# Kernel optimization log

Measured on AMD Instinct MI355X. Metric: run time of the kernel, lower is better.

The kernel has to match this reference:

```python
import jax, jax.numpy as jnp
import numpy as np

N = 100000
E = 1600000
IN_DIM = 64
H_DIM = 64
OUT_DIM = 1


def gcn_conv(x, edge_index, W, b):
    """PyG-style GCNConv: D^-1/2 (A + I) D^-1/2 X W + b."""
    n = x.shape[0]
    h = x @ W  # [N, h]
    src, dst = edge_index[0], edge_index[1]
    # degree with self-loops
    deg = jax.ops.segment_sum(jnp.ones(src.shape[0], x.dtype), dst, num_segments=n) + 1.0
    dinv = jax.lax.rsqrt(deg)  # deg >= 1 always (self-loops)
    # neighbor messages, symmetric normalization
    coef = dinv[src] * dinv[dst]                       # [E]
    msg = h[src] * coef[:, None]                       # [E, h]
    agg = jax.ops.segment_sum(msg, dst, num_segments=n)
    # self-loop contribution
    agg = agg + h * (dinv * dinv)[:, None]
    return agg + b


def setup_inputs() -> dict:
    key = jax.random.key(0)
    ks = jax.random.split(key, 14)
    s = lambda d: 1.0 / np.sqrt(d)
    return {
        "x": jax.random.normal(ks[0], (N, IN_DIM), jnp.float32),
        "edge_index": jax.random.randint(ks[1], (2, E), 0, N, jnp.int64),
        "fake_x": jax.random.normal(ks[2], (N, IN_DIM), jnp.float32),
        "fake_edge_index": jax.random.randint(ks[3], (2, E), 0, N, jnp.int64),
        "W1": jax.random.uniform(ks[4], (IN_DIM, H_DIM), jnp.float32, -s(IN_DIM), s(IN_DIM)),
        "b1": jnp.zeros((H_DIM,), jnp.float32),
        "W2": jax.random.uniform(ks[5], (H_DIM, H_DIM), jnp.float32, -s(H_DIM), s(H_DIM)),
        "b2": jnp.zeros((H_DIM,), jnp.float32),
        "Wy": jax.random.uniform(ks[6], (H_DIM, OUT_DIM), jnp.float32, -s(H_DIM), s(H_DIM)),
        "by": jnp.zeros((OUT_DIM,), jnp.float32),
        "Wp": jax.random.uniform(ks[7], (H_DIM, OUT_DIM), jnp.float32, -s(H_DIM), s(H_DIM)),
        "bp": jnp.zeros((OUT_DIM,), jnp.float32),
        "Wb": jax.random.uniform(ks[8], (H_DIM, OUT_DIM), jnp.float32, -s(H_DIM), s(H_DIM)),
        "bb": jnp.zeros((OUT_DIM,), jnp.float32),
    }


def reference(x, edge_index, fake_x, fake_edge_index,
              W1, b1, W2, b2, Wy, by, Wp, bp, Wb, bb):
    # eval mode: dropout is identity
    xZ1 = jax.nn.relu(gcn_conv(x, edge_index, W1, b1))
    xfZ1 = jax.nn.relu(gcn_conv(fake_x, fake_edge_index, W1, b1))
    xZ2 = gcn_conv(xZ1, edge_index, W2, b2)
    xfZ2 = gcn_conv(xfZ1, fake_edge_index, W2, b2)
    yi = jax.nn.relu(xZ2 @ Wy + by)
    fprob = jax.nn.relu(xZ2 @ Wp + bp)
    fprob_f = jax.nn.relu(xfZ2 @ Wp + bp)
    treat_prob = jax.nn.relu(xZ2 @ Wb + bb)
    return (yi, fprob, fprob_f, treat_prob)
```

## Files before the change

kernel.cpp:

```cpp
#include <hip/hip_runtime.h>
#include <hip/hip_bf16.h>

typedef __hip_bfloat16 bf16;

__device__ __forceinline__ float b2f(bf16 v) { return __bfloat162float(v); }
__device__ __forceinline__ float bu2f(unsigned short u) { return __uint_as_float(((unsigned)u) << 16); }
__device__ __forceinline__ unsigned short f2bu(float f) {
    bf16 h = __float2bfloat16(f);
    return *(unsigned short*)&h;
}

__device__ __forceinline__ int getIdx(const void* p, long long i, int is64) {
    return is64 ? (int)(((const long long*)p)[i]) : ((const int*)p)[i];
}
__device__ __forceinline__ float loadF(const void* p, size_t i, int isF32) {
    return isF32 ? ((const float*)p)[i] : b2f(((const bf16*)p)[i]);
}
__device__ __forceinline__ void storeF(void* p, size_t i, float v, int isF32) {
    if (isF32) ((float*)p)[i] = v;
    else       ((bf16*)p)[i]  = __float2bfloat16(v);
}

#define NPART 128
#define CHUNK 2048
#define BINCAP 40
#define MAXSLICE 800

__global__ void setup_kernel(const void* __restrict__ edge, const void* __restrict__ x,
                             const void* __restrict__ b2, const void* __restrict__ W2,
                             const void* __restrict__ Wy, const void* __restrict__ by,
                             const void* __restrict__ Wp, const void* __restrict__ bp,
                             const void* __restrict__ Wb, const void* __restrict__ bb,
                             float* __restrict__ c, int* __restrict__ flags,
                             int* __restrict__ bCntAll) {
    __shared__ int sh_isF32;
    const int tid  = threadIdx.x;
    const int lane = tid & 63;
    const int wv   = tid >> 6;
    bCntAll[tid] = 0;
    if (wv == 0) {
        const int* e32 = (const int*)edge;
        int nz = 0;
        for (int k = 1 + 2 * lane; k < 1024; k += 128) nz |= (e32[k] != 0);
        int allzero = !__any(nz);
        if (allzero) {
            int nz2 = 0;
            for (int k = 1000001 + 2 * lane; k < 1002048; k += 128) nz2 |= (e32[k] != 0);
            allzero = !__any(nz2);
        }
        const unsigned short* u = (const unsigned short*)x;
        int insane = 0;
        for (int k = 2 * lane; k < 512; k += 128) {
            int ex = (u[k] >> 7) & 0xFF;
            if (ex != 0 && (ex < 90 || ex > 160)) insane++;
        }
#pragma unroll
        for (int off = 32; off > 0; off >>= 1) insane += __shfl_xor(insane, off, 64);
        if (lane == 0) {
            flags[0] = allzero;
            flags[1] = (insane > 64) ? 1 : 0;
            sh_isF32 = (insane > 64) ? 1 : 0;
        }
    }
    __syncthreads();
    const int isF32 = sh_isF32;
    if (wv == 0) {
        float b = loadF(b2, lane, isF32);
        float cy = b * loadF(Wy, lane, isF32);
        float cp = b * loadF(Wp, lane, isF32);
        float cb = b * loadF(Wb, lane, isF32);
#pragma unroll
        for (int off = 32; off > 0; off >>= 1) {
            cy += __shfl_xor(cy, off, 64);
            cp += __shfl_xor(cp, off, 64);
            cb += __shfl_xor(cb, off, 64);
        }
        if (lane == 0) {
            c[0] = cy + loadF(by, 0, isF32);
            c[1] = cp + loadF(bp, 0, isF32);
            c[2] = cb + loadF(bb, 0, isF32);
        }
    } else {
        const void* Wh = (wv == 1) ? Wy : (wv == 2) ? Wp : Wb;
        float* dst = c + 16 + (wv - 1) * 64;
        float acc = 0.f;
        for (int j = 0; j < 64; ++j)
            acc = fmaf(loadF(W2, (size_t)lane * 64 + j, isF32), loadF(Wh, j, isF32), acc);
        dst[lane] = acc;
    }
}

__global__ void bucket_kernel(const void* __restrict__ e0, const void* __restrict__ e1,
                              int E, int N,
                              unsigned* __restrict__ bk0, unsigned* __restrict__ bk1,
                              int bucketCap, int* __restrict__ bCntBase,
                              const int* __restrict__ flags) {
    __shared__ unsigned bins[NPART][BINCAP];
    __shared__ int binCnt[NPART];
    __shared__ int binBase[NPART];
    const int g = blockIdx.y;
    const void* edge = g ? e1 : e0;
    unsigned* __restrict__ bucket = g ? bk1 : bk0;
    int* __restrict__ bCnt = bCntBase + g * NPART;
    const int is64 = flags[0];
    const int tid = threadIdx.x;
    long long base = (long long)blockIdx.x * CHUNK;
    if (base >= E) return;
    if (tid < NPART) binCnt[tid] = 0;
    __syncthreads();
    for (int k = tid; k < CHUNK; k += 256) {
        long long e = base + k;
        if (e < E) {
            int s = getIdx(edge, e, is64);
            int d = getIdx(edge, (long long)E + e, is64);
            int p = (int)(((long long)d * NPART) / N);
            if (p > NPART - 1) p = NPART - 1;
            int lo = (int)(((long long)N * p + NPART - 1) / NPART);
            unsigned packed = ((unsigned)s << 10) | (unsigned)(d - lo);
            int idx = atomicAdd(&binCnt[p], 1);
            if (idx < BINCAP) bins[p][idx] = packed;
            else {
                int pos = atomicAdd(&bCnt[p], 1);
                bucket[(size_t)p * bucketCap + pos] = packed;
            }
        }
    }
    __syncthreads();
    if (tid < NPART) {
        int cnt = min(binCnt[tid], BINCAP);
        binBase[tid] = atomicAdd(&bCnt[tid], cnt);
        binCnt[tid]  = cnt;
    }
    __syncthreads();
    for (int p = 0; p < NPART; ++p) {
        int cnt = binCnt[p];
        int gb  = binBase[p];
        unsigned* dstp = bucket + (size_t)p * bucketCap + gb;
        for (int k = tid; k < cnt; k += 256) dstp[k] = bins[p][k];
    }
}

__global__ void csr_build_kernel(const unsigned* __restrict__ bk0, const unsigned* __restrict__ bk1,
                                 int bucketCap, const int* __restrict__ bCntBase,
                                 int* __restrict__ rp0, int* __restrict__ rp1,
                                 float* __restrict__ dv0, float* __restrict__ dv1,
                                 int* __restrict__ cs0, int* __restrict__ cs1,
                                 int N, int E) {
    __shared__ int hist[MAXSLICE];
    __shared__ int tmp[1024];
    __shared__ int partBase;
    const int g = blockIdx.y;
    const unsigned* __restrict__ bucket = g ? bk1 : bk0;
    const int* __restrict__ bCnt = bCntBase + g * NPART;
    int*   __restrict__ rowptr  = g ? rp1 : rp0;
    float* __restrict__ dinv    = g ? dv1 : dv0;
    int*   __restrict__ csr_src = g ? cs1 : cs0;
    const int tid = threadIdx.x;
    const int p  = blockIdx.x;
    const int lo = (int)(((long long)N * p + NPART - 1) / NPART);
    const int hi = (int)(((long long)N * (p + 1) + NPART - 1) / NPART);
    const int nloc = hi - lo;
    const int cnt = bCnt[p];
    for (int t = tid; t < nloc; t += 1024) hist[t] = 0;
    if (tid == 0) {
        int b = 0;
        for (int q = 0; q < p; ++q) b += bCnt[q];
        partBase = b;
    }
    __syncthreads();
    const unsigned* __restrict__ seg = bucket + (size_t)p * bucketCap;
    for (int e = tid; e < cnt; e += 1024) atomicAdd(&hist[seg[e] & 1023u], 1);
    __syncthreads();
    const int k0 = tid * 2;
    const int s0 = (k0     < nloc) ? hist[k0]     : 0;
    const int s1 = (k0 + 1 < nloc) ? hist[k0 + 1] : 0;
    tmp[tid] = s0 + s1;
    __syncthreads();
#pragma unroll
    for (int off = 1; off < 1024; off <<= 1) {
        int v = (tid >= off) ? tmp[tid - off] : 0;
        __syncthreads();
        tmp[tid] += v;
        __syncthreads();
    }
    const int r0 = partBase + tmp[tid] - (s0 + s1);
    if (k0 < nloc) {
        rowptr[lo + k0] = r0;
        dinv[lo + k0]   = rsqrtf((float)s0 + 1.0f);
        hist[k0] = r0;
    }
    if (k0 + 1 < nloc) {
        rowptr[lo + k0 + 1] = r0 + s0;
        dinv[lo + k0 + 1]   = rsqrtf((float)s1 + 1.0f);
        hist[k0 + 1] = r0 + s0;
    }
    if (p == NPART - 1 && tid == 0) rowptr[N] = E;
    __syncthreads();
    int e = tid;
    for (; e + 3 * 1024 < cnt; e += 4 * 1024) {
        unsigned v0 = seg[e];
        unsigned v1 = seg[e + 1024];
        unsigned v2 = seg[e + 2048];
        unsigned v3 = seg[e + 3072];
        csr_src[atomicAdd(&hist[v0 & 1023u], 1)] = (int)(v0 >> 10);
        csr_src[atomicAdd(&hist[v1 & 1023u], 1)] = (int)(v1 >> 10);
        csr_src[atomicAdd(&hist[v2 & 1023u], 1)] = (int)(v2 >> 10);
        csr_src[atomicAdd(&hist[v3 & 1023u], 1)] = (int)(v3 >> 10);
    }
    for (; e < cnt; e += 1024) {
        unsigned v = seg[e];
        csr_src[atomicAdd(&hist[v & 1023u], 1)] = (int)(v >> 10);
    }
}

#define XSTR 68

__global__ void gemm64_kernel(const void* __restrict__ in0, const void* __restrict__ in1,
                              const void* __restrict__ W,
                              const float* __restrict__ dv0, const float* __restrict__ dv1,
                              unsigned short* __restrict__ o0, unsigned short* __restrict__ o1,
                              int N, const int* __restrict__ flags) {
    __shared__ float Wl[64 * 64];
    __shared__ float Xl[64 * XSTR];
    const int g = blockIdx.y;
    const void* __restrict__ in = g ? in1 : in0;
    const float* __restrict__ dinv = g ? dv1 : dv0;
    unsigned short* __restrict__ out = g ? o1 : o0;
    const int isF32 = flags[1];
    const int tid = threadIdx.x;
    if (isF32) {
        const float4* W4 = (const float4*)W;
        float4* Wl4 = (float4*)Wl;
        for (int t = tid; t < 64 * 16; t += 256) Wl4[t] = W4[t];
    } else {
        for (int t = tid; t < 64 * 64; t += 256) Wl[t] = b2f(((const bf16*)W)[t]);
    }
    const int lane = tid & 63;
    const int wave = tid >> 6;
    const int slot = lane >> 4;
    const int fi   = lane & 15;
    const int r0   = wave * 16 + slot;

    for (int base = blockIdx.x * 64; base < N; base += gridDim.x * 64) {
        __syncthreads();
        if (isF32) {
            const float4* in4 = (const float4*)in;
            for (int t = tid; t < 64 * 16; t += 256) {
                int r = t >> 4, c4 = t & 15;
                int gr = base + r;
                float4 v = (gr < N) ? in4[(size_t)gr * 16 + c4] : make_float4(0.f, 0.f, 0.f, 0.f);
                *(float4*)&Xl[r * XSTR + c4 * 4] = v;
            }
        } else {
            for (int t = tid; t < 64 * 64; t += 256) {
                int r = t >> 6, c = t & 63;
                int gr = base + r;
                Xl[r * XSTR + c] = (gr < N) ? b2f(((const bf16*)in)[(size_t)gr * 64 + c]) : 0.f;
            }
        }
        __syncthreads();

        float4 a0 = make_float4(0.f,0.f,0.f,0.f), a1 = a0, a2 = a0, a3 = a0;
#pragma unroll 2
        for (int k = 0; k < 64; k += 4) {
            float4 w0 = *(const float4*)&Wl[(k + 0) * 64 + fi * 4];
            float4 w1 = *(const float4*)&Wl[(k + 1) * 64 + fi * 4];
            float4 w2 = *(const float4*)&Wl[(k + 2) * 64 + fi * 4];
            float4 w3 = *(const float4*)&Wl[(k + 3) * 64 + fi * 4];
            float4 x0 = *(const float4*)&Xl[(r0 +  0) * XSTR + k];
            float4 x1 = *(const float4*)&Xl[(r0 +  4) * XSTR + k];
            float4 x2 = *(const float4*)&Xl[(r0 +  8) * XSTR + k];
            float4 x3 = *(const float4*)&Xl[(r0 + 12) * XSTR + k];
            a0.x=fmaf(x0.x,w0.x,a0.x); a0.y=fmaf(x0.x,w0.y,a0.y); a0.z=fmaf(x0.x,w0.z,a0.z); a0.w=fmaf(x0.x,w0.w,a0.w);
            a0.x=fmaf(x0.y,w1.x,a0.x); a0.y=fmaf(x0.y,w1.y,a0.y); a0.z=fmaf(x0.y,w1.z,a0.z); a0.w=fmaf(x0.y,w1.w,a0.w);
            a0.x=fmaf(x0.z,w2.x,a0.x); a0.y=fmaf(x0.z,w2.y,a0.y); a0.z=fmaf(x0.z,w2.z,a0.z); a0.w=fmaf(x0.z,w2.w,a0.w);
            a0.x=fmaf(x0.w,w3.x,a0.x); a0.y=fmaf(x0.w,w3.y,a0.y); a0.z=fmaf(x0.w,w3.z,a0.z); a0.w=fmaf(x0.w,w3.w,a0.w);
            a1.x=fmaf(x1.x,w0.x,a1.x); a1.y=fmaf(x1.x,w0.y,a1.y); a1.z=fmaf(x1.x,w0.z,a1.z); a1.w=fmaf(x1.x,w0.w,a1.w);
            a1.x=fmaf(x1.y,w1.x,a1.x); a1.y=fmaf(x1.y,w1.y,a1.y); a1.z=fmaf(x1.y,w1.z,a1.z); a1.w=fmaf(x1.y,w1.w,a1.w);
            a1.x=fmaf(x1.z,w2.x,a1.x); a1.y=fmaf(x1.z,w2.y,a1.y); a1.z=fmaf(x1.z,w2.z,a1.z); a1.w=fmaf(x1.z,w2.w,a1.w);
            a1.x=fmaf(x1.w,w3.x,a1.x); a1.y=fmaf(x1.w,w3.y,a1.y); a1.z=fmaf(x1.w,w3.z,a1.z); a1.w=fmaf(x1.w,w3.w,a1.w);
            a2.x=fmaf(x2.x,w0.x,a2.x); a2.y=fmaf(x2.x,w0.y,a2.y); a2.z=fmaf(x2.x,w0.z,a2.z); a2.w=fmaf(x2.x,w0.w,a2.w);
            a2.x=fmaf(x2.y,w1.x,a2.x); a2.y=fmaf(x2.y,w1.y,a2.y); a2.z=fmaf(x2.y,w1.z,a2.z); a2.w=fmaf(x2.y,w1.w,a2.w);
            a2.x=fmaf(x2.z,w2.x,a2.x); a2.y=fmaf(x2.z,w2.y,a2.y); a2.z=fmaf(x2.z,w2.z,a2.z); a2.w=fmaf(x2.z,w2.w,a2.w);
            a2.x=fmaf(x2.w,w3.x,a2.x); a2.y=fmaf(x2.w,w3.y,a2.y); a2.z=fmaf(x2.w,w3.z,a2.z); a2.w=fmaf(x2.w,w3.w,a2.w);
            a3.x=fmaf(x3.x,w0.x,a3.x); a3.y=fmaf(x3.x,w0.y,a3.y); a3.z=fmaf(x3.x,w0.z,a3.z); a3.w=fmaf(x3.x,w0.w,a3.w);
            a3.x=fmaf(x3.y,w1.x,a3.x); a3.y=fmaf(x3.y,w1.y,a3.y); a3.z=fmaf(x3.y,w1.z,a3.z); a3.w=fmaf(x3.y,w1.w,a3.w);
            a3.x=fmaf(x3.z,w2.x,a3.x); a3.y=fmaf(x3.z,w2.y,a3.y); a3.z=fmaf(x3.z,w2.z,a3.z); a3.w=fmaf(x3.z,w2.w,a3.w);
            a3.x=fmaf(x3.w,w3.x,a3.x); a3.y=fmaf(x3.w,w3.y,a3.y); a3.z=fmaf(x3.w,w3.z,a3.z); a3.w=fmaf(x3.w,w3.w,a3.w);
        }
        float4 acc[4] = {a0, a1, a2, a3};
#pragma unroll
        for (int j = 0; j < 4; ++j) {
            int r = base + r0 + 4 * j;
            if (r < N) {
                float d = dinv[r];
                ushort4 o;
                o.x = f2bu(acc[j].x * d); o.y = f2bu(acc[j].y * d);
                o.z = f2bu(acc[j].z * d); o.w = f2bu(acc[j].w * d);
                ((ushort4*)out)[(size_t)r * 16 + fi] = o;
            }
        }
    }
}

__global__ void gather_fused_kernel(const int* __restrict__ cs0, const int* __restrict__ cs1,
                                    const int* __restrict__ rp0, const int* __restrict__ rp1,
                                    const float* __restrict__ dv0, const float* __restrict__ dv1,
                                    const unsigned short* __restrict__ hp0, const unsigned short* __restrict__ hp1,
                                    const void* __restrict__ bias, const float* __restrict__ cv,
                                    float4* __restrict__ t40, float4* __restrict__ t41,
                                    int N, const int* __restrict__ flags) {
    const int g = blockIdx.y;
    const int* __restrict__ csr_src = g ? cs1 : cs0;
    const int* __restrict__ rowptr  = g ? rp1 : rp0;
    const float* __restrict__ dinv  = g ? dv1 : dv0;
    const unsigned short* __restrict__ hp = g ? hp1 : hp0;
    float4* __restrict__ t4 = g ? t41 : t40;
    const int isF32 = flags[1];
    const int lane = threadIdx.x & 63;
    const int slot = lane >> 4;
    const int fi   = lane & 15;
    const int i = blockIdx.x * (blockDim.x >> 6) + (threadIdx.x >> 6);
    if (i >= N) return;
    const ushort4* __restrict__ h4 = (const ushort4*)hp;
    const int beg = rowptr[i];
    const int end = rowptr[i + 1];
    const int hsel = (slot < 3) ? slot : 0;
    float4 w4 = *(const float4*)&cv[16 + hsel * 64 + fi * 4];
    float4 bias4;
    if (isF32) bias4 = ((const float4*)bias)[fi];
    else {
        ushort4 ub = ((const ushort4*)bias)[fi];
        bias4 = make_float4(bu2f(ub.x), bu2f(ub.y), bu2f(ub.z), bu2f(ub.w));
    }

    float4 a0 = make_float4(0.f, 0.f, 0.f, 0.f);
    float4 a1 = make_float4(0.f, 0.f, 0.f, 0.f);
    float4 a2 = make_float4(0.f, 0.f, 0.f, 0.f);
    float4 a3 = make_float4(0.f, 0.f, 0.f, 0.f);
    int e = beg + slot;
    for (; e + 12 < end; e += 16) {
        int s0 = csr_src[e];
        int s1 = csr_src[e + 4];
        int s2 = csr_src[e + 8];
        int s3 = csr_src[e + 12];
        ushort4 u0 = h4[(size_t)s0 * 16 + fi];
        ushort4 u1 = h4[(size_t)s1 * 16 + fi];
        ushort4 u2 = h4[(size_t)s2 * 16 + fi];
        ushort4 u3 = h4[(size_t)s3 * 16 + fi];
        a0.x += bu2f(u0.x); a0.y += bu2f(u0.y); a0.z += bu2f(u0.z); a0.w += bu2f(u0.w);
        a1.x += bu2f(u1.x); a1.y += bu2f(u1.y); a1.z += bu2f(u1.z); a1.w += bu2f(u1.w);
        a2.x += bu2f(u2.x); a2.y += bu2f(u2.y); a2.z += bu2f(u2.z); a2.w += bu2f(u2.w);
        a3.x += bu2f(u3.x); a3.y += bu2f(u3.y); a3.z += bu2f(u3.z); a3.w += bu2f(u3.w);
    }
    for (; e < end; e += 4) {
        int s = csr_src[e];
        ushort4 u = h4[(size_t)s * 16 + fi];
        a0.x += bu2f(u.x); a0.y += bu2f(u.y); a0.z += bu2f(u.z); a0.w += bu2f(u.w);
    }
    a0.x += a1.x + a2.x + a3.x; a0.y += a1.y + a2.y + a3.y;
    a0.z += a1.z + a2.z + a3.z; a0.w += a1.w + a2.w + a3.w;
    a0.x += __shfl_xor(a0.x, 16, 64); a0.y += __shfl_xor(a0.y, 16, 64);
    a0.z += __shfl_xor(a0.z, 16, 64); a0.w += __shfl_xor(a0.w, 16, 64);
    a0.x += __shfl_xor(a0.x, 32, 64); a0.y += __shfl_xor(a0.y, 32, 64);
    a0.z += __shfl_xor(a0.z, 32, 64); a0.w += __shfl_xor(a0.w, 32, 64);

    const float di = dinv[i];
    ushort4 ui = h4[(size_t)i * 16 + fi];
    float4 v;
    v.x = fmaxf(fmaf(a0.x + bu2f(ui.x), di, bias4.x), 0.f);
    v.y = fmaxf(fmaf(a0.y + bu2f(ui.y), di, bias4.y), 0.f);
    v.z = fmaxf(fmaf(a0.z + bu2f(ui.z), di, bias4.z), 0.f);
    v.w = fmaxf(fmaf(a0.w + bu2f(ui.w), di, bias4.w), 0.f);

    float t = v.x * w4.x + v.y * w4.y + v.z * w4.z + v.w * w4.w;
#pragma unroll
    for (int off = 1; off < 16; off <<= 1) t += __shfl_xor(t, off, 64);
    if (fi == 0 && slot < 3) ((float*)(t4 + i))[slot] = t * di;
}

__global__ void gather_scalar_kernel(const int* __restrict__ cs0, const int* __restrict__ cs1,
                                     const int* __restrict__ rp0, const int* __restrict__ rp1,
                                     const float* __restrict__ dv0, const float* __restrict__ dv1,
                                     const float4* __restrict__ t40, const float4* __restrict__ t41,
                                     const float* __restrict__ c, void* __restrict__ out,
                                     int N, int gbase, const int* __restrict__ flags) {
    const int g = blockIdx.y;
    const int* __restrict__ csr_src = g ? cs1 : cs0;
    const int* __restrict__ rowptr  = g ? rp1 : rp0;
    const float* __restrict__ dinv  = g ? dv1 : dv0;
    const float4* __restrict__ t4   = g ? t41 : t40;
    const int mode = gbase + g;
    int tid  = blockIdx.x * blockDim.x + threadIdx.x;
    int i    = tid >> 2;
    int slot = tid & 3;
    if (i >= N) return;
    const int beg = rowptr[i];
    const int end = rowptr[i + 1];
    float ax = 0.f, ay = 0.f, az = 0.f;
    for (int e = beg + slot; e < end; e += 4) {
        float4 t = t4[csr_src[e]];
        ax += t.x; ay += t.y; az += t.z;
    }
    ax += __shfl_xor(ax, 1, 64); ay += __shfl_xor(ay, 1, 64); az += __shfl_xor(az, 1, 64);
    ax += __shfl_xor(ax, 2, 64); ay += __shfl_xor(ay, 2, 64); az += __shfl_xor(az, 2, 64);
    if (slot == 0) {
        const int isF32 = flags[1];
        float4 ti = t4[i];
        float di  = dinv[i];
        if (mode == 0) {
            storeF(out, (size_t)i,         fmaxf(fmaf(di, ax + ti.x, c[0]), 0.0f), isF32);
            storeF(out, (size_t)N + i,     fmaxf(fmaf(di, ay + ti.y, c[1]), 0.0f), isF32);
            storeF(out, (size_t)3 * N + i, fmaxf(fmaf(di, az + ti.z, c[2]), 0.0f), isF32);
        } else {
            storeF(out, (size_t)2 * N + i, fmaxf(fmaf(di, ay + ti.y, c[1]), 0.0f), isF32);
        }
    }
}

extern "C" void kernel_launch(void* const* d_in, const int* in_sizes, int n_in,
                              void* d_out, int out_size, void* d_ws, size_t ws_size,
                              hipStream_t stream) {
    const void* x   = d_in[0];
    const void* ei  = d_in[1];
    const void* fx  = d_in[2];
    const void* fei = d_in[3];
    const void* W1  = d_in[4];
    const void* b1  = d_in[5];
    const void* W2  = d_in[6];
    const void* b2  = d_in[7];
    const void* Wy  = d_in[8];
    const void* by  = d_in[9];
    const void* Wp  = d_in[10];
    const void* bp  = d_in[11];
    const void* Wb  = d_in[12];
    const void* bb  = d_in[13];

    const int N = in_sizes[0] / 64;
    const int E = in_sizes[1] / 2;
    const int bucketCap = E / NPART + 2048;

    char* base = (char*)d_ws;
    int dup = 2;
    int *flags = nullptr, *bCnt = nullptr;
    int *rp[2], *cs[2];
    unsigned* bk[2];
    float* dv[2];
    float* cvals = nullptr;
    unsigned short* bA[2];
    float4* t4[2];

    for (int attempt = 0; attempt < 2; ++attempt) {
        size_t off = 0;
        auto alloc = [&](size_t bytes) { size_t r = (off + 15) & ~(size_t)15; off = r + bytes; return r; };
        size_t o_flags = alloc(16 * 4);
        size_t o_bcnt  = alloc(2 * NPART * 4);
        size_t o_rp[2], o_cs[2], o_bk[2], o_dv[2], o_bA[2], o_t4[2], o_cv;
        for (int g = 0; g < dup; ++g) o_rp[g] = alloc((size_t)(N + 1) * 4);
        for (int g = 0; g < dup; ++g) o_cs[g] = alloc((size_t)E * 4);
        for (int g = 0; g < dup; ++g) o_bk[g] = alloc((size_t)NPART * bucketCap * 4);
        for (int g = 0; g < dup; ++g) o_dv[g] = alloc((size_t)N * 4);
        o_cv = alloc((16 + 192) * 4);
        for (int g = 0; g < dup; ++g) o_bA[g] = alloc((size_t)N * 64 * 2);
        for (int g = 0; g < dup; ++g) o_t4[g] = alloc((size_t)N * 16);
        if (off > ws_size && dup == 2) { dup = 1; continue; }
        flags = (int*)(base + o_flags);
        bCnt  = (int*)(base + o_bcnt);
        cvals = (float*)(base + o_cv);
        for (int g = 0; g < 2; ++g) {
            int s = (g < dup) ? g : 0;
            rp[g] = (int*)(base + o_rp[s]);
            cs[g] = (int*)(base + o_cs[s]);
            bk[g] = (unsigned*)(base + o_bk[s]);
            dv[g] = (float*)(base + o_dv[s]);
            bA[g] = (unsigned short*)(base + o_bA[s]);
            t4[g] = (float4*)(base + o_t4[s]);
        }
        break;
    }

    const int THREADS = 256;
    const int nChunks = (E + CHUNK - 1) / CHUNK;
    const int nTiles  = (N + 63) / 64;
    const int nScal   = (4 * N + THREADS - 1) / THREADS;
    const int nGather = (N + 3) / 4;

    setup_kernel<<<1, 256, 0, stream>>>(ei, x, b2, W2, Wy, by, Wp, bp, Wb, bb, cvals, flags, bCnt);

    if (dup == 2) {
        bucket_kernel<<<dim3(nChunks, 2), THREADS, 0, stream>>>(
            ei, fei, E, N, bk[0], bk[1], bucketCap, bCnt, flags);
        csr_build_kernel<<<dim3(NPART, 2), 1024, 0, stream>>>(
            bk[0], bk[1], bucketCap, bCnt, rp[0], rp[1], dv[0], dv[1], cs[0], cs[1], N, E);
        gemm64_kernel<<<dim3(nTiles, 2), THREADS, 0, stream>>>(
            x, fx, W1, dv[0], dv[1], bA[0], bA[1], N, flags);
        gather_fused_kernel<<<dim3(nGather, 2), THREADS, 0, stream>>>(
            cs[0], cs[1], rp[0], rp[1], dv[0], dv[1], bA[0], bA[1], b1, cvals,
            t4[0], t4[1], N, flags);
        gather_scalar_kernel<<<dim3(nScal, 2), THREADS, 0, stream>>>(
            cs[0], cs[1], rp[0], rp[1], dv[0], dv[1], t4[0], t4[1], cvals, d_out, N, 0, flags);
    } else {
        for (int g = 0; g < 2; ++g) {
            const void* xg   = g ? fx : x;
            const void* edge = g ? fei : ei;
            int* bCntg = bCnt + g * NPART;
            bucket_kernel<<<dim3(nChunks, 1), THREADS, 0, stream>>>(
                edge, edge, E, N, bk[0], bk[0], bucketCap, bCntg, flags);
            csr_build_kernel<<<dim3(NPART, 1), 1024, 0, stream>>>(
                bk[0], bk[0], bucketCap, bCntg, rp[0], rp[0], dv[0], dv[0], cs[0], cs[0], N, E);
            gemm64_kernel<<<dim3(nTiles, 1), THREADS, 0, stream>>>(
                xg, xg, W1, dv[0], dv[0], bA[0], bA[0], N, flags);
            gather_fused_kernel<<<dim3(nGather, 1), THREADS, 0, stream>>>(
                cs[0], cs[0], rp[0], rp[0], dv[0], dv[0], bA[0], bA[0], b1, cvals,
                t4[0], t4[0], N, flags);
            gather_scalar_kernel<<<dim3(nScal, 1), THREADS, 0, stream>>>(
                cs[0], cs[0], rp[0], rp[0], dv[0], dv[0], t4[0], t4[0], cvals, d_out, N, g, flags);
        }
    }
}
```

Baseline: 366.0 us.

## Flatten bucket flush, parallel-scan partition bases, widen scalar gather to 16 lanes

The bucket kernel's per-partition flush loop, which left most threads idle on small bins, is replaced by a block-wide prefix scan of bin counts. Each thread then binary-searches the scan to copy a flat range of elements. csr_build computes each partition's base offset with a parallel shared-memory scan instead of a serial loop in thread 0. The scalar gather now gives each node 16 lanes instead of 4, with a matching shuffle reduction and grid size, to increase memory-level parallelism on neighbor loads. The cost is extra barriers and binary-search work, plus idle lanes for low-degree nodes.

```diff
diff --git a/kernel.cpp b/kernel.cpp
--- a/kernel.cpp
+++ b/kernel.cpp
@@ -98,6 +98,7 @@
     __shared__ unsigned bins[NPART][BINCAP];
     __shared__ int binCnt[NPART];
     __shared__ int binBase[NPART];
+    __shared__ int pfx[NPART];
     const int g = blockIdx.y;
     const void* edge = g ? e1 : e0;
     unsigned* __restrict__ bucket = g ? bk1 : bk0;
@@ -130,13 +131,23 @@
         int cnt = min(binCnt[tid], BINCAP);
         binBase[tid] = atomicAdd(&bCnt[tid], cnt);
         binCnt[tid]  = cnt;
-    }
-    __syncthreads();
-    for (int p = 0; p < NPART; ++p) {
-        int cnt = binCnt[p];
-        int gb  = binBase[p];
-        unsigned* dstp = bucket + (size_t)p * bucketCap + gb;
-        for (int k = tid; k < cnt; k += 256) dstp[k] = bins[p][k];
+        pfx[tid]     = cnt;
+    }
+    __syncthreads();
+    for (int off = 1; off < NPART; off <<= 1) {
+        int v = 0;
+        if (tid < NPART && tid >= off) v = pfx[tid - off];
+        __syncthreads();
+        if (tid < NPART) pfx[tid] += v;
+        __syncthreads();
+    }
+    const int total = pfx[NPART - 1];
+    for (int k = tid; k < total; k += 256) {
+        int lo2 = 0, hi2 = NPART - 1;
+        while (lo2 < hi2) { int mid = (lo2 + hi2) >> 1; if (pfx[mid] > k) hi2 = mid; else lo2 = mid + 1; }
+        int p = lo2;
+        int idx = k - (p ? pfx[p - 1] : 0);
+        bucket[(size_t)p * bucketCap + binBase[p] + idx] = bins[p][idx];
     }
 }
 
@@ -148,7 +159,7 @@
                                  int N, int E) {
     __shared__ int hist[MAXSLICE];
     __shared__ int tmp[1024];
-    __shared__ int partBase;
+    __shared__ int sc[NPART];
     const int g = blockIdx.y;
     const unsigned* __restrict__ bucket = g ? bk1 : bk0;
     const int* __restrict__ bCnt = bCntBase + g * NPART;
@@ -162,12 +173,16 @@
     const int nloc = hi - lo;
     const int cnt = bCnt[p];
     for (int t = tid; t < nloc; t += 1024) hist[t] = 0;
-    if (tid == 0) {
-        int b = 0;
-        for (int q = 0; q < p; ++q) b += bCnt[q];
-        partBase = b;
-    }
-    __syncthreads();
+    if (tid < NPART) sc[tid] = bCnt[tid];
+    __syncthreads();
+    for (int off = 1; off < NPART; off <<= 1) {
+        int v = 0;
+        if (tid < NPART && tid >= off) v = sc[tid - off];
+        __syncthreads();
+        if (tid < NPART) sc[tid] += v;
+        __syncthreads();
+    }
+    const int partBase = sc[p] - cnt;
     const unsigned* __restrict__ seg = bucket + (size_t)p * bucketCap;
     for (int e = tid; e < cnt; e += 1024) atomicAdd(&hist[seg[e] & 1023u], 1);
     __syncthreads();
@@ -391,20 +406,23 @@
     const float* __restrict__ dinv  = g ? dv1 : dv0;
     const float4* __restrict__ t4   = g ? t41 : t40;
     const int mode = gbase + g;
-    int tid  = blockIdx.x * blockDim.x + threadIdx.x;
-    int i    = tid >> 2;
-    int slot = tid & 3;
+    const int li = threadIdx.x & 15;
+    const int i  = blockIdx.x * (blockDim.x >> 4) + (threadIdx.x >> 4);
     if (i >= N) return;
     const int beg = rowptr[i];
     const int end = rowptr[i + 1];
     float ax = 0.f, ay = 0.f, az = 0.f;
-    for (int e = beg + slot; e < end; e += 4) {
+    for (int e = beg + li; e < end; e += 16) {
         float4 t = t4[csr_src[e]];
         ax += t.x; ay += t.y; az += t.z;
     }
-    ax += __shfl_xor(ax, 1, 64); ay += __shfl_xor(ay, 1, 64); az += __shfl_xor(az, 1, 64);
-    ax += __shfl_xor(ax, 2, 64); ay += __shfl_xor(ay, 2, 64); az += __shfl_xor(az, 2, 64);
-    if (slot == 0) {
+#pragma unroll
+    for (int off = 1; off < 16; off <<= 1) {
+        ax += __shfl_xor(ax, off, 64);
+        ay += __shfl_xor(ay, off, 64);
+        az += __shfl_xor(az, off, 64);
+    }
+    if (li == 0) {
         const int isF32 = flags[1];
         float4 ti = t4[i];
         float di  = dinv[i];
@@ -482,7 +500,7 @@
     const int THREADS = 256;
     const int nChunks = (E + CHUNK - 1) / CHUNK;
     const int nTiles  = (N + 63) / 64;
-    const int nScal   = (4 * N + THREADS - 1) / THREADS;
+    const int nScal   = (N + 15) / 16;
     const int nGather = (N + 3) / 4;
 
     setup_kernel<<<1, 256, 0, stream>>>(ei, x, b2, W2, Wy, by, Wp, bp, Wb, bb, cvals, flags, bCnt);
```

After: 344.5 us (median of 2 runs). 1.06x faster.
